# Kernel tuning notes

Measured on AMD Instinct MI355X. Metric: run time of the kernel, lower is better.

Reference implementation:

```python
import jax, jax.numpy as jnp
import numpy as np

PH = PW = 8
HEADS = 8
ADIM = 256
DH = ADIM // HEADS
N_KEYS = 3
CK, CV, CQ = 16, 32, 16
KS = 7
K_PDIM = PH * PW * CK   # 1024
V_PDIM = PH * PW * CV   # 2048
Q_PDIM = PH * PW * CQ   # 1024
MB_IN = N_KEYS * CV     # 96
MB_HID = 4 * MB_IN      # 384


def _to_patches(x):
    # b c (h ph) (w pw) -> b (h w) (ph pw c)
    b, c, H, W = x.shape
    h, w = H // PH, W // PW
    x = x.reshape(b, c, h, PH, w, PW).transpose(0, 2, 4, 3, 5, 1)
    return x.reshape(b, h * w, PH * PW * c)


def _layernorm(x, g, b):
    m = x.mean(-1, keepdims=True)
    v = x.var(-1, keepdims=True)
    return (x - m) * jax.lax.rsqrt(v + 1e-5) * g + b


def _embed(x, W1, b1, W2, b2):
    # NonLinearEmbedding: Linear -> GELU -> Linear
    return jax.nn.gelu(x @ W1 + b1) @ W2 + b2


def _to_heads(x):
    # b n (h d) -> b h n d
    b, n, hd = x.shape
    return x.reshape(b, n, HEADS, hd // HEADS).transpose(0, 2, 1, 3)


def _conv(x, w, b, groups, pad):
    y = jax.lax.conv_general_dilated(
        x, w, (1, 1), pad,
        dimension_numbers=('NCHW', 'OIHW', 'NCHW'),
        feature_group_count=groups)
    return y + b[None, :, None, None]


def _mbconv(x, w_exp, b_exp, w_dw, b_dw, w_proj, b_proj):
    # grouped 1x1 expand -> GELU -> depthwise kxk -> GELU -> grouped 1x1 project
    h = jax.nn.gelu(_conv(x, w_exp, b_exp, HEADS, 'VALID'))
    h = jax.nn.gelu(_conv(h, w_dw, b_dw, MB_HID, 'SAME'))
    return _conv(h, w_proj, b_proj, HEADS, 'VALID')


def setup_inputs() -> dict:
    key = jax.random.key(0)
    ks = jax.random.split(key, 24)
    B = 2
    key_sizes = [(256, 256), (192, 320), (128, 128)]
    query_sizes = [(256, 256), (192, 192)]
    s = 0.02
    inp = {}
    for i, (h, w) in enumerate(key_sizes):
        inp[f'keys_{i}'] = jax.random.normal(ks[i], (B, CK, h, w), jnp.float32)
        inp[f'values_{i}'] = jax.random.normal(ks[3 + i], (B, CV, h, w), jnp.float32)
    for i, (h, w) in enumerate(query_sizes):
        inp[f'queries_{i}'] = jax.random.normal(ks[6 + i], (B, CQ, h, w), jnp.float32)
    inp['ln_g'] = jnp.ones((V_PDIM,), jnp.float32)
    inp['ln_b'] = jnp.zeros((V_PDIM,), jnp.float32)
    inp['kW1'] = jax.random.normal(ks[8], (K_PDIM, ADIM), jnp.float32) * s
    inp['kb1'] = jnp.zeros((ADIM,), jnp.float32)
    inp['kW2'] = jax.random.normal(ks[9], (ADIM, ADIM), jnp.float32) * s
    inp['kb2'] = jnp.zeros((ADIM,), jnp.float32)
    inp['qW1'] = jax.random.normal(ks[10], (Q_PDIM, ADIM), jnp.float32) * s
    inp['qb1'] = jnp.zeros((ADIM,), jnp.float32)
    inp['qW2'] = jax.random.normal(ks[11], (ADIM, ADIM), jnp.float32) * s
    inp['qb2'] = jnp.zeros((ADIM,), jnp.float32)
    inp['w_exp'] = jax.random.normal(ks[12], (MB_HID, MB_IN // HEADS, 1, 1), jnp.float32) * s
    inp['b_exp'] = jnp.zeros((MB_HID,), jnp.float32)
    inp['w_dw'] = jax.random.normal(ks[13], (MB_HID, 1, KS, KS), jnp.float32) * s
    inp['b_dw'] = jnp.zeros((MB_HID,), jnp.float32)
    inp['w_proj'] = jax.random.normal(ks[14], (CV, MB_HID // HEADS, 1, 1), jnp.float32) * s
    inp['b_proj'] = jnp.zeros((CV,), jnp.float32)
    return inp


def reference(keys_0, keys_1, keys_2, values_0, values_1, values_2,
              queries_0, queries_1, ln_g, ln_b, kW1, kb1, kW2, kb2,
              qW1, qb1, qW2, qb2, w_exp, b_exp, w_dw, b_dw, w_proj, b_proj):
    keys = [keys_0, keys_1, keys_2]
    values = [values_0, values_1, values_2]
    queries = [queries_0, queries_1]
    # spatial sizes are already multiples of (PH, PW) -> pad_to_next_multiple is identity
    query_sizes = [q.shape[-2:] for q in queries]
    kp = [_to_patches(k) for k in keys]
    vp = [_to_patches(v) for v in values]
    qp = [_to_patches(q) for q in queries]
    nk = [p.shape[1] for p in kp]
    nq = [p.shape[1] for p in qp]
    k_seq = jnp.concatenate(kp, axis=1)               # (b, Nk, K_PDIM)
    v_seq = _layernorm(jnp.concatenate(vp, axis=1), ln_g, ln_b)  # (b, Nk, V_PDIM)
    q_seq = jnp.concatenate(qp, axis=1)               # (b, Nq, Q_PDIM)
    k_emb = _to_heads(_embed(k_seq, kW1, kb1, kW2, kb2))  # (b, h, Nk, DH)
    q_emb = _to_heads(_embed(q_seq, qW1, qb1, qW2, qb2))  # (b, h, Nq, DH)
    v_h = _to_heads(v_seq)                                # (b, h, Nk, dv)
    scale = jnp.asarray(1.0 / np.sqrt(DH), k_emb.dtype)
    attn = jnp.einsum('bhid,bhjd->bhij', q_emb, k_emb) * scale
    attn = jax.nn.softmax(attn, axis=-1)
    offs = np.cumsum([0] + nk)
    # per-source weighted values, stacked along a new source axis k
    weighted = jnp.stack(
        [attn[..., offs[i]:offs[i + 1]] @ v_h[:, :, offs[i]:offs[i + 1]]
         for i in range(N_KEYS)], axis=1)              # (b, k, h, Nq, dv)
    qoffs = np.cumsum([0] + nq)
    outs = []
    c = CV // HEADS
    for i, (qh, qw) in enumerate(query_sizes):
        v = weighted[:, :, :, qoffs[i]:qoffs[i + 1]]   # (b, k, hd, n, d)
        b, k, hd, n, d = v.shape
        h, w = qh // PH, qw // PW
        # b k hd (h w) (ph pw c) -> b (hd k c) (h ph) (w pw)
        v = v.reshape(b, k, hd, h, w, PH, PW, c).transpose(0, 2, 1, 7, 3, 5, 4, 6)
        v = v.reshape(b, hd * k * c, h * PH, w * PW)
        outs.append(_mbconv(v, w_exp, b_exp, w_dw, b_dw, w_proj, b_proj))
    return tuple(outs)
```

## Files before the change

### kernel.cpp

```cpp
#include <hip/hip_runtime.h>
#include <hip/hip_bf16.h>
#include <math.h>

typedef unsigned short bfu;
typedef __attribute__((ext_vector_type(8))) short short8v;
typedef __attribute__((ext_vector_type(4))) float f32x4;
typedef __attribute__((ext_vector_type(2))) float f32x2;

__device__ __forceinline__ float fast_rcp(float d) {
    float r = __builtin_amdgcn_rcpf(d);
    return r * fmaf(-d, r, 2.0f);
}
__device__ __forceinline__ f32x2 fma2(f32x2 a, f32x2 b, f32x2 c) {
    return __builtin_elementwise_fma(a, b, c);
}
__device__ __forceinline__ f32x2 splat2(float w) { return (f32x2){w, w}; }
__device__ __forceinline__ float gelu_f(float x) {
    float x3 = x * x * x;
    float e = __expf(1.5957691f * fmaf(0.044715f, x3, x));
    return x * e * __builtin_amdgcn_rcpf(e + 1.0f);
}
__device__ __forceinline__ f32x2 gelu2(f32x2 x) {
    f32x2 x3 = x * x * x;
    f32x2 z = fma2(splat2(0.044715f), x3, x) * 1.5957691f;
    f32x2 e = {__expf(z.x), __expf(z.y)};
    f32x2 d = e + 1.0f;
    f32x2 r = {__builtin_amdgcn_rcpf(d.x), __builtin_amdgcn_rcpf(d.y)};
    return x * e * r;
}
__device__ __forceinline__ float bf2f(bfu u) {
    union { float f; unsigned int i; } v; v.i = ((unsigned int)u) << 16; return v.f;
}
__device__ __forceinline__ bfu f2bf(float f) {
    union { float f; unsigned int i; } v; v.f = f;
    unsigned int r = v.i + 0x7fff + ((v.i >> 16) & 1);
    return (bfu)(r >> 16);
}
__device__ __forceinline__ float ldin(const void* p, size_t i, bool f32) {
    return f32 ? ((const float*)p)[i] : bf2f(((const bfu*)p)[i]);
}
__device__ __forceinline__ void stout(void* p, size_t i, float v, bool f32) {
    if (f32) ((float*)p)[i] = v;
    else     ((bfu*)p)[i] = f2bf(v);
}
__device__ __forceinline__ short8v ld_frag8(const bfu* p) {
    union { short8v v; ushort4 u[2]; } t;
    t.u[0] = *(const ushort4*)p;
    t.u[1] = *(const ushort4*)(p + 4);
    return t.v;
}

__global__ __launch_bounds__(256) void detect_kernel(const void* probe, int* flag) {
    __shared__ int red[4];
    const bfu* p = (const bfu*)probe;
    int tid = threadIdx.x;
    int insane = 0;
    for (int i = tid; i < 2048; i += 256) {
        unsigned e = (p[i] >> 7) & 0xFF;
        if (e >= 0xC0 || (e != 0 && e < 0x40)) insane++;
    }
    for (int o = 32; o > 0; o >>= 1) insane += __shfl_down(insane, o);
    if ((tid & 63) == 0) red[tid >> 6] = insane;
    __syncthreads();
    if (tid == 0) flag[0] = (red[0] + red[1] + red[2] + red[3] > 64) ? 1 : 0;
}

__global__ __launch_bounds__(256) void zero_out_kernel(bfu* __restrict__ out, int n) {
    int i = blockIdx.x * 256 + threadIdx.x;
    if (i < n) out[i] = 0;
}

__global__ __launch_bounds__(256) void wprep_kernel(
    const void* __restrict__ wexp, const void* __restrict__ bexp,
    const void* __restrict__ wdw, const void* __restrict__ bdw,
    const void* __restrict__ wproj, const void* __restrict__ bproj,
    const int* __restrict__ flag, float* __restrict__ wf)
{
    bool f32 = flag[0] != 0;
    int i = blockIdx.x * 256 + threadIdx.x;
    if (i < 4608)       wf[i] = ldin(wexp, i, f32);
    else if (i < 4992)  wf[i] = ldin(bexp, i - 4608, f32);
    else if (i < 23808) wf[i] = ldin(wdw, i - 4992, f32);
    else if (i < 24192) wf[i] = ldin(bdw, i - 23808, f32);
    else if (i < 25728) wf[i] = ldin(wproj, i - 24192, f32);
    else if (i < 25760) wf[i] = ldin(bproj, i - 25728, f32);
}

__global__ __launch_bounds__(256) void ln_stats_kernel(
    const void* __restrict__ v0, const void* __restrict__ v1, const void* __restrict__ v2,
    const int* __restrict__ flag, float* __restrict__ m_buf, float* __restrict__ i_buf)
{
    __shared__ float red[16];
    bool f32 = flag[0] != 0;
    int bid = blockIdx.x;
    int b = bid / 2240, n = bid - b * 2240;
    const void* src; int nl, wp, H, W;
    if (n < 1024)      { src = v0; nl = n;        wp = 32; H = 256; W = 256; }
    else if (n < 1984) { src = v1; nl = n - 1024; wp = 40; H = 192; W = 320; }
    else               { src = v2; nl = n - 1984; wp = 16; H = 128; W = 128; }
    int tid = threadIdx.x;
    int py = nl / wp, px = nl - py * wp;
    int ybase = py * 8, xbase = px * 8;
    float s1 = 0.f, s2 = 0.f;
    #pragma unroll
    for (int i = 0; i < 8; i++) {
        int j = tid + 256 * i;
        int ph = j >> 8, pw = (j >> 5) & 7, c = j & 31;
        float v = ldin(src, ((size_t)(b * 32 + c) * H + ybase + ph) * W + xbase + pw, f32);
        s1 += v; s2 = fmaf(v, v, s2);
    }
    for (int o = 32; o > 0; o >>= 1) { s1 += __shfl_down(s1, o); s2 += __shfl_down(s2, o); }
    int wid = tid >> 6;
    if ((tid & 63) == 0) { red[wid] = s1; red[8 + wid] = s2; }
    __syncthreads();
    if (tid == 0) {
        float a = red[0] + red[1] + red[2] + red[3];
        float q = red[8] + red[9] + red[10] + red[11];
        float m = a * (1.0f / 2048.0f);
        float var = q * (1.0f / 2048.0f) - m * m;
        m_buf[bid] = m;
        i_buf[bid] = 1.0f / sqrtf(var + 1e-5f);
    }
}

__global__ __launch_bounds__(256) void vstage_kernel(
    const void* __restrict__ v0, const void* __restrict__ v1, const void* __restrict__ v2,
    const void* __restrict__ g, const void* __restrict__ beta,
    const int* __restrict__ flag, bfu* __restrict__ out)
{
    __shared__ float red[16];
    __shared__ float mv[2];
    __shared__ __align__(16) bfu Ls[2048];
    bool f32 = flag[0] != 0;
    int bid = blockIdx.x;
    int b = bid / 2240, n = bid - b * 2240;
    const void* src; int nl, wpn, H, W;
    if (n < 1024)      { src = v0; nl = n;        wpn = 32; H = 256; W = 256; }
    else if (n < 1984) { src = v1; nl = n - 1024; wpn = 40; H = 192; W = 320; }
    else               { src = v2; nl = n - 1984; wpn = 16; H = 128; W = 128; }
    int tid = threadIdx.x;
    int py = nl / wpn, px = nl - py * wpn;
    int p = tid & 63;
    int c0 = tid >> 6;
    int y = py * 8 + (p >> 3), x = px * 8 + (p & 7);
    size_t HW = (size_t)H * W;
    size_t base = ((size_t)(b * 32 + c0) * H + y) * W + x;
    float vals[8];
    float s1 = 0.f, s2 = 0.f;
    #pragma unroll
    for (int i = 0; i < 8; i++) {
        float v = ldin(src, base + (size_t)(i << 2) * HW, f32);
        vals[i] = v; s1 += v; s2 = fmaf(v, v, s2);
    }
    for (int o = 32; o > 0; o >>= 1) { s1 += __shfl_down(s1, o); s2 += __shfl_down(s2, o); }
    int wid = tid >> 6;
    if ((tid & 63) == 0) { red[wid] = s1; red[8 + wid] = s2; }
    __syncthreads();
    if (tid == 0) {
        float a = red[0] + red[1] + red[2] + red[3];
        float q = red[8] + red[9] + red[10] + red[11];
        float m = a * (1.0f / 2048.0f);
        float var = q * (1.0f / 2048.0f) - m * m;
        mv[0] = m; mv[1] = 1.0f / sqrtf(var + 1e-5f);
    }
    __syncthreads();
    float m = mv[0], inv = mv[1];
    int jb = (p >> 3) * 256 + (p & 7) * 32 + c0;
    #pragma unroll
    for (int i = 0; i < 8; i++) {
        int j = jb + (i << 2);
        float o = (vals[i] - m) * inv * ldin(g, j, f32) + ldin(beta, j, f32);
        Ls[j] = f2bf(o);
    }
    __syncthreads();
    short8v* dst = (short8v*)(out + (size_t)bid * 2048);
    dst[tid] = ((const short8v*)Ls)[tid];
}

__global__ __launch_bounds__(256) void vtr_kernel(
    const bfu* __restrict__ vseq, bfu* __restrict__ vT)
{
    __shared__ __align__(16) bfu Ls[17408];
    int bid = blockIdx.x;
    int ch = bid % 35;
    int t = bid / 35;
    int h = t & 7, b = t >> 3;
    int c = threadIdx.x;
    const bfu* srcb = vseq + (((size_t)(b * 2240 + (ch << 6))) << 11) + (h << 8) + c;
    #pragma unroll
    for (int k4 = 0; k4 < 16; k4++) {
        ushort4 v;
        v.x = srcb[(size_t)(k4 * 4 + 0) << 11];
        v.y = srcb[(size_t)(k4 * 4 + 1) << 11];
        v.z = srcb[(size_t)(k4 * 4 + 2) << 11];
        v.w = srcb[(size_t)(k4 * 4 + 3) << 11];
        *(ushort4*)&Ls[c * 68 + k4 * 4] = v;
    }
    __syncthreads();
    short8v* dst = (short8v*)(vT + (size_t)((b * 8 + h) * 35 + ch) * 17408);
    const short8v* s = (const short8v*)Ls;
    #pragma unroll
    for (int r = 0; r < 8; r++) dst[(r << 8) + c] = s[(r << 8) + c];
    if (c < 128) dst[2048 + c] = s[2048 + c];
}

__global__ __launch_bounds__(256) void kstage_kernel(
    const void* __restrict__ k0, const void* __restrict__ k1, const void* __restrict__ k2,
    const void* __restrict__ q0, const void* __restrict__ q1,
    const int* __restrict__ flag, bfu* __restrict__ k_seq, bfu* __restrict__ q_seq)
{
    bool f32 = flag[0] != 0;
    int tid = threadIdx.x;
    int w = tid >> 6, l = tid & 63;
    int row = blockIdx.x * 4 + w;
    const void* src; int b, nl, wpn, H, W; bfu* dst;
    if (row < 4480) {
        b = row / 2240; int n = row - b * 2240;
        if (n < 1024)      { src = k0; nl = n;        wpn = 32; H = 256; W = 256; }
        else if (n < 1984) { src = k1; nl = n - 1024; wpn = 40; H = 192; W = 320; }
        else               { src = k2; nl = n - 1984; wpn = 16; H = 128; W = 128; }
        dst = k_seq + ((size_t)row << 10);
    } else {
        int r2 = row - 4480;
        b = r2 / 1600; int n = r2 - b * 1600;
        if (n < 1024)      { src = q0; nl = n;        wpn = 32; H = 256; W = 256; }
        else               { src = q1; nl = n - 1024; wpn = 24; H = 192; W = 192; }
        dst = q_seq + ((size_t)r2 << 10);
    }
    int py = nl / wpn, px = nl - py * wpn;
    int y = (py << 3) + (l >> 3), x = (px << 3) + (l & 7);
    size_t HW = (size_t)H * W;
    size_t base = ((size_t)(b * 16) * H + y) * W + x;
    bfu vals[16];
    #pragma unroll
    for (int c = 0; c < 16; c++) vals[c] = f2bf(ldin(src, base + c * HW, f32));
    bfu* dp = dst + (l << 4);
    *(ushort4*)(dp + 0)  = *(ushort4*)&vals[0];
    *(ushort4*)(dp + 4)  = *(ushort4*)&vals[4];
    *(ushort4*)(dp + 8)  = *(ushort4*)&vals[8];
    *(ushort4*)(dp + 12) = *(ushort4*)&vals[12];
}

__global__ __launch_bounds__(256) void wstage_kernel(
    const void* __restrict__ kW1, const void* __restrict__ qW1,
    const void* __restrict__ kW2, const void* __restrict__ qW2,
    const void* __restrict__ kb1, const void* __restrict__ qb1,
    const void* __restrict__ kb2, const void* __restrict__ qb2,
    const int* __restrict__ flag, bfu* __restrict__ WT, float* __restrict__ biasf)
{
    __shared__ float Ls[64][65];
    bool f32 = flag[0] != 0;
    int bid = blockIdx.x;
    int tid = threadIdx.x;
    if (bid == 160) {
        biasf[tid]       = ldin(kb1, tid, f32);
        biasf[256 + tid] = ldin(qb1, tid, f32);
        biasf[512 + tid] = ldin(kb2, tid, f32);
        biasf[768 + tid] = ldin(qb2, tid, f32);
        return;
    }
    const void* src; bfu* dst; int K, t;
    if (bid < 64)       { src = kW1; dst = WT;          K = 1024; t = bid; }
    else if (bid < 128) { src = qW1; dst = WT + 262144; K = 1024; t = bid - 64; }
    else if (bid < 144) { src = kW2; dst = WT + 524288; K = 256;  t = bid - 128; }
    else                { src = qW2; dst = WT + 589824; K = 256;  t = bid - 144; }
    int ktiles = K >> 6;
    int tk = t % ktiles, tc = t / ktiles;
    int k0 = tk << 6, c0 = tc << 6;
    int j = tid & 63, i0 = tid >> 6;
    #pragma unroll
    for (int p = 0; p < 16; p++) {
        int i = i0 + (p << 2);
        Ls[j][i] = ldin(src, (size_t)(k0 + i) * 256 + c0 + j, f32);
    }
    __syncthreads();
    #pragma unroll
    for (int p = 0; p < 16; p++) {
        int ci = i0 + (p << 2);
        dst[(size_t)(c0 + ci) * K + k0 + j] = f2bf(Ls[ci][j]);
    }
}

__global__ __launch_bounds__(256) void embed_mfma_kernel(
    const bfu* __restrict__ Ak, const bfu* __restrict__ Aq,
    const bfu* __restrict__ WTk, const bfu* __restrict__ WTq,
    const float* __restrict__ bk, const float* __restrict__ bq,
    bfu* __restrict__ Ck, bfu* __restrict__ Cq,
    int K, int gelu, int tiles0)
{
    int bid = blockIdx.x;
    int c0 = (bid & 3) << 6;
    int rt = bid >> 2;
    const bfu* A; const bfu* WT; const float* bias; bfu* C;
    int row0;
    if (rt < tiles0) { A = Ak; WT = WTk; bias = bk; C = Ck; row0 = rt << 6; }
    else             { A = Aq; WT = WTq; bias = bq; C = Cq; row0 = (rt - tiles0) << 6; }
    int tid = threadIdx.x;
    int w = tid >> 6, l = tid & 63;
    int l15 = l & 15, g = l >> 4;
    f32x4 zero4 = {0.f, 0.f, 0.f, 0.f};
    f32x4 acc[4] = {zero4, zero4, zero4, zero4};
    const bfu* wp = WT + (size_t)(c0 + (w << 4) + l15) * K + (g << 3);
    const bfu* ap = A + (size_t)(row0 + l15) * K + (g << 3);
    int nk = K >> 5;
    for (int kk = 0; kk < nk; kk++) {
        short8v af = ld_frag8(wp + (kk << 5));
        #pragma unroll
        for (int r2 = 0; r2 < 4; r2++) {
            short8v bf = ld_frag8(ap + (size_t)(r2 << 4) * K + (kk << 5));
            acc[r2] = __builtin_amdgcn_mfma_f32_16x16x32_bf16(af, bf, acc[r2], 0, 0, 0);
        }
    }
    int colb = c0 + (w << 4) + (g << 2);
    float4 bb = *(const float4*)&bias[colb];
    #pragma unroll
    for (int r2 = 0; r2 < 4; r2++) {
        float v0 = acc[r2][0] + bb.x;
        float v1 = acc[r2][1] + bb.y;
        float v2 = acc[r2][2] + bb.z;
        float v3 = acc[r2][3] + bb.w;
        if (gelu) { v0 = gelu_f(v0); v1 = gelu_f(v1); v2 = gelu_f(v2); v3 = gelu_f(v3); }
        ushort4 o;
        o.x = f2bf(v0); o.y = f2bf(v1); o.z = f2bf(v2); o.w = f2bf(v3);
        *(ushort4*)(C + (size_t)(row0 + (r2 << 4) + l15) * 256 + colb) = o;
    }
}

__global__ __launch_bounds__(256) void embed1_kernel(
    const void* __restrict__ k0, const void* __restrict__ k1, const void* __restrict__ k2,
    const void* __restrict__ q0, const void* __restrict__ q1,
    const void* __restrict__ kW1, const void* __restrict__ kb1,
    const void* __restrict__ qW1, const void* __restrict__ qb1,
    const int* __restrict__ flag,
    bfu* __restrict__ k_hid, bfu* __restrict__ q_hid)
{
    __shared__ float As[16][68];
    __shared__ float Bs[16][68];
    bool f32 = flag[0] != 0;
    int bid = blockIdx.x;
    int colBase = (bid & 3) << 6;
    int rt = bid >> 2;
    const void* Wm; const void* bias; bfu* C;
    int rowBase, isK;
    if (rt < 70) { isK = 1; Wm = kW1; bias = kb1; C = k_hid; rowBase = rt << 6; }
    else         { isK = 0; Wm = qW1; bias = qb1; C = q_hid; rowBase = (rt - 70) << 6; }
    int tid = threadIdx.x;
    int tx = tid & 15, ty = tid >> 4;
    int arow = tid >> 2, akq = (tid & 3) << 2;
    int brow = tid >> 4, bcol = (tid & 15) << 2;
    int row = rowBase + arow;
    int nTot = isK ? 2240 : 1600;
    int b = row / nTot, n = row - b * nTot;
    const void* src; int nl, wp, H, W;
    if (isK) {
        if (n < 1024)      { src = k0; nl = n;        wp = 32; H = 256; W = 256; }
        else if (n < 1984) { src = k1; nl = n - 1024; wp = 40; H = 192; W = 320; }
        else               { src = k2; nl = n - 1984; wp = 16; H = 128; W = 128; }
    } else {
        if (n < 1024)      { src = q0; nl = n;        wp = 32; H = 256; W = 256; }
        else               { src = q1; nl = n - 1024; wp = 24; H = 192; W = 192; }
    }
    int py = nl / wp, px = nl - py * wp;
    int ybase = py << 3, xbase = px << 3;
    size_t HW = (size_t)H * W;
    size_t abase = (size_t)(b * 16 + akq) * HW;
    size_t wbase = (size_t)brow * 256 + colBase + bcol;
    float acc[4][4] = {};
    for (int k0i = 0; k0i < 1024; k0i += 16) {
        int j = k0i + akq;
        int ph = j >> 7, pw = (j >> 4) & 7;
        size_t ai = abase + (size_t)(ybase + ph) * W + xbase + pw;
        As[akq + 0][arow] = ldin(src, ai, f32);
        As[akq + 1][arow] = ldin(src, ai + HW, f32);
        As[akq + 2][arow] = ldin(src, ai + 2 * HW, f32);
        As[akq + 3][arow] = ldin(src, ai + 3 * HW, f32);
        size_t wo = wbase + (size_t)k0i * 256;
        #pragma unroll
        for (int t = 0; t < 4; t++) Bs[brow][bcol + t] = ldin(Wm, wo + t, f32);
        __syncthreads();
        #pragma unroll
        for (int kk = 0; kk < 16; kk++) {
            float4 a4 = *(const float4*)&As[kk][ty << 2];
            float4 p0 = *(const float4*)&Bs[kk][tx << 2];
            float ar[4] = {a4.x, a4.y, a4.z, a4.w};
            float br[4] = {p0.x, p0.y, p0.z, p0.w};
            #pragma unroll
            for (int rr = 0; rr < 4; rr++)
                #pragma unroll
                for (int i = 0; i < 4; i++)
                    acc[rr][i] = fmaf(ar[rr], br[i], acc[rr][i]);
        }
        __syncthreads();
    }
    int cg = colBase + (tx << 2);
    float bbr[4];
    #pragma unroll
    for (int i = 0; i < 4; i++) bbr[i] = ldin(bias, cg + i, f32);
    #pragma unroll
    for (int rr = 0; rr < 4; rr++) {
        ushort4 o;
        o.x = f2bf(gelu_f(acc[rr][0] + bbr[0]));
        o.y = f2bf(gelu_f(acc[rr][1] + bbr[1]));
        o.z = f2bf(gelu_f(acc[rr][2] + bbr[2]));
        o.w = f2bf(gelu_f(acc[rr][3] + bbr[3]));
        *(ushort4*)(&C[(size_t)(rowBase + (ty << 2) + rr) * 256 + cg]) = o;
    }
}

__global__ __launch_bounds__(256) void embed2_kernel(
    const bfu* __restrict__ A0, const void* __restrict__ W0, const void* __restrict__ bias0,
    bfu* __restrict__ C0, int tiles0,
    const bfu* __restrict__ A1, const void* __restrict__ W1, const void* __restrict__ bias1,
    bfu* __restrict__ C1, const int* __restrict__ flag)
{
    __shared__ float As[16][68];
    __shared__ float Bs[16][68];
    bool f32 = flag[0] != 0;
    int bid = blockIdx.x;
    int colBase = (bid & 3) << 6;
    int rt = bid >> 2;
    const bfu* A; const void* Wm; const void* bias; bfu* C;
    int rowBase;
    if (rt < tiles0) { A = A0; Wm = W0; bias = bias0; C = C0; rowBase = rt << 6; }
    else             { A = A1; Wm = W1; bias = bias1; C = C1; rowBase = (rt - tiles0) << 6; }
    int tid = threadIdx.x;
    int tx = tid & 15, ty = tid >> 4;
    int arow = tid >> 2, akq = (tid & 3) << 2;
    int brow = tid >> 4, bcol = (tid & 15) << 2;
    const bfu* Ap = A + (size_t)(rowBase + arow) * 256 + akq;
    size_t wbase = (size_t)brow * 256 + colBase + bcol;
    float acc[4][4] = {};
    for (int k0 = 0; k0 < 256; k0 += 16) {
        ushort4 av = *(const ushort4*)(Ap + k0);
        As[akq + 0][arow] = bf2f(av.x);
        As[akq + 1][arow] = bf2f(av.y);
        As[akq + 2][arow] = bf2f(av.z);
        As[akq + 3][arow] = bf2f(av.w);
        size_t wo = wbase + (size_t)k0 * 256;
        #pragma unroll
        for (int t = 0; t < 4; t++) Bs[brow][bcol + t] = ldin(Wm, wo + t, f32);
        __syncthreads();
        #pragma unroll
        for (int kk = 0; kk < 16; kk++) {
            float4 a4 = *(const float4*)&As[kk][ty << 2];
            float4 p0 = *(const float4*)&Bs[kk][tx << 2];
            float ar[4] = {a4.x, a4.y, a4.z, a4.w};
            float br[4] = {p0.x, p0.y, p0.z, p0.w};
            #pragma unroll
            for (int rr = 0; rr < 4; rr++)
                #pragma unroll
                for (int i = 0; i < 4; i++)
                    acc[rr][i] = fmaf(ar[rr], br[i], acc[rr][i]);
        }
        __syncthreads();
    }
    int cg = colBase + (tx << 2);
    float bbr[4];
    #pragma unroll
    for (int i = 0; i < 4; i++) bbr[i] = ldin(bias, cg + i, f32);
    #pragma unroll
    for (int rr = 0; rr < 4; rr++) {
        ushort4 o;
        o.x = f2bf(acc[rr][0] + bbr[0]);
        o.y = f2bf(acc[rr][1] + bbr[1]);
        o.z = f2bf(acc[rr][2] + bbr[2]);
        o.w = f2bf(acc[rr][3] + bbr[3]);
        *(ushort4*)(&C[(size_t)(rowBase + (ty << 2) + rr) * 256 + cg]) = o;
    }
}

__global__ __launch_bounds__(256) void attn_mfma_kernel(
    const bfu* __restrict__ qe, const bfu* __restrict__ ke,
    const bfu* __restrict__ vT,
    bfu* __restrict__ wbuf, float* __restrict__ lbuf, int h0, int hs)
{
    __shared__ __align__(16) bfu Vs[17408];
    __shared__ __align__(16) bfu Ps[2176];
    __shared__ float red[4][16];
    int bid = blockIdx.x;
    int qtile = bid % 50;
    int t = bid / 50;
    int hh = t % hs, b = t / hs;
    int h = h0 + hh;
    int n0 = qtile << 5;
    int tid = threadIdx.x;
    int w = tid >> 6, l = tid & 63;
    int l15 = l & 15, g = l >> 4;
    int wqt = w >> 1;
    int wkp = (w & 1) << 1;

    short8v qf = *(const short8v*)(qe + (((size_t)(b * 1600 + n0 + (wqt << 4) + l15)) << 8) + (h << 5) + (g << 3));

    f32x4 zero4 = {0.f, 0.f, 0.f, 0.f};
    f32x4 acc[2][4];
    #pragma unroll
    for (int i = 0; i < 2; i++)
        #pragma unroll
        for (int j = 0; j < 4; j++) acc[i][j] = zero4;
    float rs = 0.f;
    const float scale = 0.17677669529663687f;

    const short8v* vbase = (const short8v*)(vT + (size_t)((b * 8 + h) * 35) * 17408);
    short8v* VsV = (short8v*)Vs;

    for (int ch = 0; ch < 35; ch++) {
        const short8v* src = vbase + (size_t)ch * 2176;
        #pragma unroll
        for (int r = 0; r < 8; r++) VsV[(r << 8) + tid] = src[(r << 8) + tid];
        if (tid < 128) VsV[2048 + tid] = src[2048 + tid];
        #pragma unroll
        for (int j = 0; j < 2; j++) {
            int ktile = wkp + j;
            short8v kf = *(const short8v*)(ke + (((size_t)(b * 2240 + (ch << 6) + (ktile << 4) + l15)) << 8) + (h << 5) + (g << 3));
            f32x4 st = __builtin_amdgcn_mfma_f32_16x16x32_bf16(kf, qf, zero4, 0, 0, 0);
            float p0 = __expf(st[0] * scale);
            float p1 = __expf(st[1] * scale);
            float p2 = __expf(st[2] * scale);
            float p3 = __expf(st[3] * scale);
            rs += (p0 + p1) + (p2 + p3);
            ushort4 pk;
            pk.x = f2bf(p0); pk.y = f2bf(p1); pk.z = f2bf(p2); pk.w = f2bf(p3);
            *(ushort4*)&Ps[((wqt << 4) + l15) * 68 + (ktile << 4) + (g << 2)] = pk;
        }
        __syncthreads();
        #pragma unroll
        for (int kt = 0; kt < 2; kt++) {
            short8v a0 = ld_frag8(&Ps[l15 * 68 + (kt << 5) + (g << 3)]);
            short8v a1 = ld_frag8(&Ps[(16 + l15) * 68 + (kt << 5) + (g << 3)]);
            #pragma unroll
            for (int nt = 0; nt < 4; nt++) {
                int ntg = (w << 2) + nt;
                short8v bf = ld_frag8(&Vs[((ntg << 4) + l15) * 68 + (kt << 5) + (g << 3)]);
                acc[0][nt] = __builtin_amdgcn_mfma_f32_16x16x32_bf16(a0, bf, acc[0][nt], 0, 0, 0);
                acc[1][nt] = __builtin_amdgcn_mfma_f32_16x16x32_bf16(a1, bf, acc[1][nt], 0, 0, 0);
            }
        }
        __syncthreads();
        if (ch == 15 || ch == 30 || ch == 34) {
            int srcid = (ch == 15) ? 0 : (ch == 30 ? 1 : 2);
            bfu* wb = wbuf + ((size_t)((b * hs + hh) * 3 + srcid) * 1600 + n0) * 256 + (w << 6) + l15;
            #pragma unroll
            for (int q2 = 0; q2 < 2; q2++)
                #pragma unroll
                for (int nt = 0; nt < 4; nt++) {
                    #pragma unroll
                    for (int r = 0; r < 4; r++) {
                        wb[(size_t)((q2 << 4) + (g << 2) + r) * 256 + (nt << 4)] = f2bf(acc[q2][nt][r]);
                        acc[q2][nt][r] = 0.f;
                    }
                }
        }
    }
    rs += __shfl_xor(rs, 16);
    rs += __shfl_xor(rs, 32);
    if (l < 16) red[w][l15] = rs;
    __syncthreads();
    if (tid < 32) {
        int q2 = tid >> 4;
        float tot = red[q2 << 1][tid & 15] + red[(q2 << 1) + 1][tid & 15];
        lbuf[(size_t)(b * 8 + h) * 1600 + n0 + tid] = tot;
    }
}

__global__ __launch_bounds__(256) void attn_kernel(
    const bfu* __restrict__ qe, const bfu* __restrict__ ke,
    const bfu* __restrict__ vseq,
    const void* __restrict__ v0, const void* __restrict__ v1, const void* __restrict__ v2,
    const void* __restrict__ ln_g, const void* __restrict__ ln_b,
    const float* __restrict__ m_buf, const float* __restrict__ i_buf,
    const int* __restrict__ flag,
    bfu* __restrict__ wbuf, float* __restrict__ lbuf, int h0, int hs)
{
    __shared__ float Qs[32][36];
    __shared__ float Ks[32][37];
    __shared__ float Ps2[32][37];
    __shared__ float Vls[32][260];
    __shared__ float gbg[256];
    __shared__ float gbb[256];
    bool f32 = flag[0] != 0;
    int bid = blockIdx.x;
    int qt = bid % 50;
    int t = bid / 50;
    int hh = t % hs;
    int b = t / hs;
    int h = h0 + hh;
    int n0 = qt << 5;
    int tid = threadIdx.x;
    int tx = tid & 15, ty = tid >> 4;
    if (!vseq) {
        gbg[tid] = ldin(ln_g, h * 256 + tid, f32);
        gbb[tid] = ldin(ln_b, h * 256 + tid, f32);
    }
    {
        int r = tid >> 3, d0 = (tid & 7) << 2;
        const bfu* qp = qe + (size_t)(b * 1600 + n0 + r) * 256 + (h << 5) + d0;
        ushort4 a = *(const ushort4*)qp;
        Qs[r][d0 + 0] = bf2f(a.x); Qs[r][d0 + 1] = bf2f(a.y);
        Qs[r][d0 + 2] = bf2f(a.z); Qs[r][d0 + 3] = bf2f(a.w);
    }
    float lreg = 0.f;
    float acc[2][4][4] = {};
    const float scale = 0.17677669529663687f;
    int kvrow = tid >> 3, kq = (tid & 7) << 2;
    const bfu* kbase = ke + (size_t)(b * 2240 + kvrow) * 256 + (h << 5) + kq;
    const bfu* vsbase = vseq ? vseq + (size_t)(b * 2240 + kvrow) * 2048 + (h << 8) + kq : nullptr;
    for (int ch = 0; ch < 70; ch++) {
        {
            ushort4 kv = *(const ushort4*)(kbase + (size_t)ch * 8192);
            Ks[kvrow][kq + 0] = bf2f(kv.x);
            Ks[kvrow][kq + 1] = bf2f(kv.y);
            Ks[kvrow][kq + 2] = bf2f(kv.z);
            Ks[kvrow][kq + 3] = bf2f(kv.w);
        }
        if (vseq) {
            #pragma unroll
            for (int i = 0; i < 8; i++) {
                ushort4 u = *(const ushort4*)(vsbase + (size_t)ch * 65536 + (i << 5));
                int d = (i << 5) + kq;
                Vls[kvrow][d + 0] = bf2f(u.x);
                Vls[kvrow][d + 1] = bf2f(u.y);
                Vls[kvrow][d + 2] = bf2f(u.z);
                Vls[kvrow][d + 3] = bf2f(u.w);
            }
        } else {
            int n = ch * 32 + kvrow;
            const void* vsrc; int nl, wp, H, W;
            if (n < 1024)      { vsrc = v0; nl = n;        wp = 32; H = 256; W = 256; }
            else if (n < 1984) { vsrc = v1; nl = n - 1024; wp = 40; H = 192; W = 320; }
            else               { vsrc = v2; nl = n - 1984; wp = 16; H = 128; W = 128; }
            int py = nl / wp, px = nl - py * wp;
            int y = py * 8 + h, xb = px * 8;
            float m = m_buf[b * 2240 + n];
            float inv = i_buf[b * 2240 + n];
            size_t HW = (size_t)H * W;
            size_t vbi = ((size_t)(b * 32 + kq) * H + y) * W + xb;
            #pragma unroll
            for (int i = 0; i < 8; i++) {
                int d = (i << 5) + kq;
                float t0 = (ldin(vsrc, vbi + i, f32) - m) * inv;
                float t1 = (ldin(vsrc, vbi + i + HW, f32) - m) * inv;
                float t2 = (ldin(vsrc, vbi + i + 2 * HW, f32) - m) * inv;
                float t3 = (ldin(vsrc, vbi + i + 3 * HW, f32) - m) * inv;
                Vls[kvrow][d + 0] = fmaf(t0, gbg[d + 0], gbb[d + 0]);
                Vls[kvrow][d + 1] = fmaf(t1, gbg[d + 1], gbb[d + 1]);
                Vls[kvrow][d + 2] = fmaf(t2, gbg[d + 2], gbb[d + 2]);
                Vls[kvrow][d + 3] = fmaf(t3, gbg[d + 3], gbb[d + 3]);
            }
        }
        __syncthreads();
        float s[2][2] = {};
        #pragma unroll 8
        for (int d = 0; d < 32; d++) {
            float k0v = Ks[(tx << 1) + 0][d];
            float k1v = Ks[(tx << 1) + 1][d];
            #pragma unroll
            for (int rr = 0; rr < 2; rr++) {
                float qv = Qs[(ty << 1) + rr][d];
                s[rr][0] = fmaf(qv, k0v, s[rr][0]);
                s[rr][1] = fmaf(qv, k1v, s[rr][1]);
            }
        }
        #pragma unroll
        for (int rr = 0; rr < 2; rr++) {
            Ps2[(ty << 1) + rr][(tx << 1) + 0] = __expf(s[rr][0] * scale);
            Ps2[(ty << 1) + rr][(tx << 1) + 1] = __expf(s[rr][1] * scale);
        }
        __syncthreads();
        if (tid < 32) {
            float t2 = 0.f;
            #pragma unroll
            for (int jj = 0; jj < 32; jj++) t2 += Ps2[tid][jj];
            lreg += t2;
        }
        #pragma unroll 4
        for (int j = 0; j < 32; j++) {
            float4 w0 = *(const float4*)&Vls[j][(tx << 2)];
            float4 w1 = *(const float4*)&Vls[j][64 + (tx << 2)];
            float4 w2 = *(const float4*)&Vls[j][128 + (tx << 2)];
            float4 w3 = *(const float4*)&Vls[j][192 + (tx << 2)];
            #pragma unroll
            for (int rr = 0; rr < 2; rr++) {
                float p = Ps2[(ty << 1) + rr][j];
                acc[rr][0][0] = fmaf(p, w0.x, acc[rr][0][0]);
                acc[rr][0][1] = fmaf(p, w0.y, acc[rr][0][1]);
                acc[rr][0][2] = fmaf(p, w0.z, acc[rr][0][2]);
                acc[rr][0][3] = fmaf(p, w0.w, acc[rr][0][3]);
                acc[rr][1][0] = fmaf(p, w1.x, acc[rr][1][0]);
                acc[rr][1][1] = fmaf(p, w1.y, acc[rr][1][1]);
                acc[rr][1][2] = fmaf(p, w1.z, acc[rr][1][2]);
                acc[rr][1][3] = fmaf(p, w1.w, acc[rr][1][3]);
                acc[rr][2][0] = fmaf(p, w2.x, acc[rr][2][0]);
                acc[rr][2][1] = fmaf(p, w2.y, acc[rr][2][1]);
                acc[rr][2][2] = fmaf(p, w2.z, acc[rr][2][2]);
                acc[rr][2][3] = fmaf(p, w2.w, acc[rr][2][3]);
                acc[rr][3][0] = fmaf(p, w3.x, acc[rr][3][0]);
                acc[rr][3][1] = fmaf(p, w3.y, acc[rr][3][1]);
                acc[rr][3][2] = fmaf(p, w3.z, acc[rr][3][2]);
                acc[rr][3][3] = fmaf(p, w3.w, acc[rr][3][3]);
            }
        }
        __syncthreads();
        if (ch == 31 || ch == 61 || ch == 69) {
            int src = (ch == 31) ? 0 : (ch == 61 ? 1 : 2);
            bfu* wb = wbuf + (size_t)(((b * hs + hh) * 3 + src) * 1600 + n0 + (ty << 1)) * 256 + (tx << 2);
            #pragma unroll
            for (int rr = 0; rr < 2; rr++) {
                #pragma unroll
                for (int q = 0; q < 4; q++) {
                    ushort4 u;
                    u.x = f2bf(acc[rr][q][0]); u.y = f2bf(acc[rr][q][1]);
                    u.z = f2bf(acc[rr][q][2]); u.w = f2bf(acc[rr][q][3]);
                    *(ushort4*)(wb + (size_t)rr * 256 + (q << 6)) = u;
                    acc[rr][q][0] = acc[rr][q][1] = acc[rr][q][2] = acc[rr][q][3] = 0.f;
                }
            }
        }
    }
    if (tid < 32) lbuf[(size_t)(b * 8 + h) * 1600 + n0 + tid] = lreg;
}

__global__ __launch_bounds__(256) void mbconv_kernel(
    const bfu* __restrict__ wbuf, const float* __restrict__ lbuf,
    const float* __restrict__ wf, const int* __restrict__ flag,
    void* __restrict__ out, size_t out_off, int H, int W, int n_base,
    int tilesX, int tilesY, int h0, int hs)
{
    __shared__ __align__(16) float h1s[8][528];
    __shared__ float h2s[256][9];
    bool f32o = flag[0] != 0;
    const float* wexp_f  = wf;
    const float* bexp_f  = wf + 4608;
    const float* wdw_f   = wf + 4992;
    const float* bdw_f   = wf + 23808;
    const float* wproj_f = wf + 24192;
    const float* bproj_f = wf + 25728;
    int bid = blockIdx.x;
    int gi = bid % hs;
    int t2b = bid / hs;
    int tilesTot = tilesX * tilesY;
    int b = t2b / tilesTot;
    int rem = t2b - b * tilesTot;
    int tY = rem / tilesX, tX = rem - tY * tilesX;
    int gy0 = tY << 4, gx0 = tX << 4;
    int wp = W >> 3;
    int tid = threadIdx.x;
    int wu = __builtin_amdgcn_readfirstlane(tid >> 6);
    int l = tid & 63;
    int doy = ((l >> 3) & 7) << 1;
    int dox = (l & 7) << 1;
    int g = h0 + gi;

    f32x2 xsr2[12];
    #pragma unroll
    for (int ci = 0; ci < 12; ci++) xsr2[ci] = (f32x2){0.f, 0.f};
    int pa0 = 0, pa1 = 0; bool pv0 = false, pv1 = false;
    bool act = tid < 242;
    if (act) {
        #pragma unroll
        for (int j = 0; j < 2; j++) {
            int p = tid * 2 + j;
            int py = p / 22, px = p - py * 22;
            int y = gy0 - 3 + py, x = gx0 - 3 + px;
            bool valid = (y >= 0) && (y < H) && (x >= 0) && (x < W);
            if (j == 0) { pa0 = py * 24 + px; pv0 = valid; }
            else        { pa1 = py * 24 + px; pv1 = valid; }
            if (valid) {
                int n = n_base + (y >> 3) * wp + (x >> 3);
                float invl = fast_rcp(lbuf[(size_t)(b * 8 + g) * 1600 + n]);
                int d = ((y & 7) << 5) + ((x & 7) << 2);
                const bfu* src = wbuf + ((size_t)((b * hs + gi) * 3) * 1600 + n) * 256 + d;
                #pragma unroll
                for (int k = 0; k < 3; k++) {
                    ushort4 u = *(const ushort4*)(src + (size_t)k * 409600);
                    if (j == 0) {
                        xsr2[k * 4 + 0].x = bf2f(u.x) * invl;
                        xsr2[k * 4 + 1].x = bf2f(u.y) * invl;
                        xsr2[k * 4 + 2].x = bf2f(u.z) * invl;
                        xsr2[k * 4 + 3].x = bf2f(u.w) * invl;
                    } else {
                        xsr2[k * 4 + 0].y = bf2f(u.x) * invl;
                        xsr2[k * 4 + 1].y = bf2f(u.y) * invl;
                        xsr2[k * 4 + 2].y = bf2f(u.z) * invl;
                        xsr2[k * 4 + 3].y = bf2f(u.w) * invl;
                    }
                }
            }
        }
    }

    float oacc[4] = {0.f, 0.f, 0.f, 0.f};
    for (int chunk = 0; chunk < 6; chunk++) {
        int hc0 = g * 48 + chunk * 8;
        __syncthreads();
        if (act) {
            #pragma unroll
            for (int c = 0; c < 8; c++) {
                const float* we = &wexp_f[(size_t)(hc0 + c) * 12];
                f32x2 a = splat2(bexp_f[hc0 + c]);
                #pragma unroll
                for (int ci = 0; ci < 12; ci++)
                    a = fma2(splat2(we[ci]), xsr2[ci], a);
                f32x2 gv = gelu2(a);
                h1s[c][pa0] = pv0 ? gv.x : 0.f;
                h1s[c][pa1] = pv1 ? gv.y : 0.f;
            }
        }
        __syncthreads();
        #pragma unroll
        for (int c2 = 0; c2 < 2; c2++) {
            int ch = wu + (c2 << 2);
            const float* wd = &wdw_f[(size_t)(hc0 + ch) * 49];
            float bd = bdw_f[hc0 + ch];
            f32x2 a2v0 = splat2(bd);
            f32x2 a2v1 = splat2(bd);
            #pragma unroll
            for (int r = 0; r < 8; r++) {
                const f32x2* rp = (const f32x2*)&h1s[ch][(doy + r) * 24 + dox];
                f32x2 p0 = rp[0], p1 = rp[1], p2 = rp[2], p3 = rp[3];
                f32x2 q0 = {p0.y, p1.x}, q1 = {p1.y, p2.x}, q2 = {p2.y, p3.x};
                f32x2 win[7] = {p0, q0, p1, q1, p2, q2, p3};
                if (r <= 6) {
                    const float* wk = &wd[r * 7];
                    #pragma unroll
                    for (int kx = 0; kx < 7; kx++)
                        a2v0 = fma2(splat2(wk[kx]), win[kx], a2v0);
                }
                if (r >= 1) {
                    const float* wk = &wd[(r - 1) * 7];
                    #pragma unroll
                    for (int kx = 0; kx < 7; kx++)
                        a2v1 = fma2(splat2(wk[kx]), win[kx], a2v1);
                }
            }
            f32x2 g0 = gelu2(a2v0), g1 = gelu2(a2v1);
            h2s[(doy + 0) * 16 + dox + 0][ch] = g0.x;
            h2s[(doy + 0) * 16 + dox + 1][ch] = g0.y;
            h2s[(doy + 1) * 16 + dox + 0][ch] = g1.x;
            h2s[(doy + 1) * 16 + dox + 1][ch] = g1.y;
        }
        __syncthreads();
        #pragma unroll
        for (int c = 0; c < 8; c++) {
            float hv = h2s[tid][c];
            #pragma unroll
            for (int oc = 0; oc < 4; oc++)
                oacc[oc] = fmaf(hv, wproj_f[(size_t)(g * 4 + oc) * 48 + chunk * 8 + c], oacc[oc]);
        }
    }
    int yy = tid >> 4, xx = tid & 15;
    #pragma unroll
    for (int oc = 0; oc < 4; oc++) {
        stout(out, out_off + ((size_t)(b * 32 + g * 4 + oc) * H + gy0 + yy) * W + gx0 + xx,
              oacc[oc] + bproj_f[g * 4 + oc], f32o);
    }
}

extern "C" void kernel_launch(void* const* d_in, const int* in_sizes, int n_in,
                              void* d_out, int out_size, void* d_ws, size_t ws_size,
                              hipStream_t stream)
{
    const void *keys0, *keys1, *keys2, *vals0, *vals1, *vals2;
    keys0 = d_in[0];
    if (in_sizes[1] == 4194304) {
        vals0 = d_in[1]; keys1 = d_in[2]; vals1 = d_in[3]; keys2 = d_in[4]; vals2 = d_in[5];
    } else {
        keys1 = d_in[1]; keys2 = d_in[2]; vals0 = d_in[3]; vals1 = d_in[4]; vals2 = d_in[5];
    }
    const void* qrys0  = d_in[6];
    const void* qrys1  = d_in[7];
    const void* ln_g   = d_in[8];
    const void* ln_b   = d_in[9];
    const void* kW1    = d_in[10];
    const void* kb1    = d_in[11];
    const void* kW2    = d_in[12];
    const void* kb2    = d_in[13];
    const void* qW1    = d_in[14];
    const void* qb1    = d_in[15];
    const void* qW2    = d_in[16];
    const void* qb2    = d_in[17];
    const void* w_exp  = d_in[18];
    const void* b_exp  = d_in[19];
    const void* w_dw   = d_in[20];
    const void* b_dw   = d_in[21];
    const void* w_proj = d_in[22];
    const void* b_proj = d_in[23];

    char* base = (char*)d_ws;
    int*   flag  = (int*)base;
    bfu*   k_emb = (bfu*)(base + 64);
    bfu*   q_emb = (bfu*)(base + 64 + 2293760);
    float* l_buf = (float*)(base + 64 + 3932160);
    float* m_buf = (float*)(base + 64 + 4034560);
    float* i_buf = (float*)(base + 64 + 4052480);
    const size_t FIXED0 = 4070464ULL;
    float* w_f   = (float*)(base + FIXED0);
    const size_t FIXEDN = FIXED0 + 103040ULL;
    const size_t VSEQB = 18350080ULL;
    const size_t VTB   = 19496960ULL;
    const size_t RX    = FIXEDN + VTB;

    const size_t EMB = 20975616ULL;
    const size_t need8 = RX + 39321600ULL;
    const size_t need4 = RX + EMB;
    const size_t need2 = RX + EMB;

    detect_kernel<<<1, 256, 0, stream>>>(keys0, flag);
    wprep_kernel<<<101, 256, 0, stream>>>(w_exp, b_exp, w_dw, b_dw, w_proj, b_proj, flag, w_f);

    if (ws_size >= need2) {
        int hs = (ws_size >= need8) ? 8 : (ws_size >= need4 ? 4 : 2);
        bfu*   vT    = (bfu*)(base + FIXEDN);
        bfu*   v_seq = (bfu*)(base + RX);
        bfu*   k_seq = (bfu*)(base + RX);
        bfu*   q_seq = (bfu*)(base + RX + 9175040);
        bfu*   WTb   = (bfu*)(base + RX + 15728640);
        float* biasf = (float*)(base + RX + 17039360);
        bfu*   k_hid = (bfu*)(base + RX + 17043456);
        bfu*   q_hid = (bfu*)(base + RX + 19337216);
        bfu*   w_buf = (bfu*)(base + RX);

        vstage_kernel<<<4480, 256, 0, stream>>>(vals0, vals1, vals2, ln_g, ln_b, flag, v_seq);
        vtr_kernel<<<560, 256, 0, stream>>>(v_seq, vT);
        kstage_kernel<<<1920, 256, 0, stream>>>(keys0, keys1, keys2, qrys0, qrys1,
                                                flag, k_seq, q_seq);
        wstage_kernel<<<161, 256, 0, stream>>>(kW1, qW1, kW2, qW2, kb1, qb1, kb2, qb2,
                                               flag, WTb, biasf);
        embed_mfma_kernel<<<480, 256, 0, stream>>>(k_seq, q_seq, WTb, WTb + 262144,
                                                   biasf, biasf + 256, k_hid, q_hid,
                                                   1024, 1, 70);
        embed_mfma_kernel<<<480, 256, 0, stream>>>(k_hid, q_hid, WTb + 524288, WTb + 589824,
                                                   biasf + 512, biasf + 768, k_emb, q_emb,
                                                   256, 0, 70);
        for (int h0 = 0; h0 < 8; h0 += hs) {
            attn_mfma_kernel<<<2 * hs * 50, 256, 0, stream>>>(
                q_emb, k_emb, vT, w_buf, l_buf, h0, hs);
            mbconv_kernel<<<2 * 256 * hs, 256, 0, stream>>>(
                w_buf, l_buf, w_f, flag,
                d_out, 0, 256, 256, 0, 16, 16, h0, hs);
            mbconv_kernel<<<2 * 144 * hs, 256, 0, stream>>>(
                w_buf, l_buf, w_f, flag,
                d_out, 4194304, 192, 192, 1024, 12, 12, h0, hs);
        }
        return;
    }

    int hs;
    if      (ws_size >= FIXEDN + 8ULL * 4915200ULL) hs = 8;
    else if (ws_size >= FIXEDN + 4ULL * 4915200ULL) hs = 4;
    else if (ws_size >= FIXEDN + 2ULL * 4915200ULL) hs = 2;
    else if (ws_size >= FIXEDN + 1ULL * 4915200ULL) hs = 1;
    else {
        zero_out_kernel<<<(out_size + 255) / 256, 256, 0, stream>>>((bfu*)d_out, out_size);
        return;
    }
    char* rest  = base + FIXEDN;
    bfu*  k_hid = (bfu*)rest;
    bfu*  q_hid = (bfu*)(rest + 2293760);
    bfu*  w_buf = (bfu*)rest;

    ln_stats_kernel<<<4480, 256, 0, stream>>>(vals0, vals1, vals2, flag, m_buf, i_buf);
    embed1_kernel<<<480, 256, 0, stream>>>(keys0, keys1, keys2, qrys0, qrys1,
                                           kW1, kb1, qW1, qb1, flag, k_hid, q_hid);
    embed2_kernel<<<480, 256, 0, stream>>>(k_hid, kW2, kb2, k_emb, 70,
                                           q_hid, qW2, qb2, q_emb, flag);
    for (int h0 = 0; h0 < 8; h0 += hs) {
        attn_kernel<<<2 * hs * 50, 256, 0, stream>>>(
            q_emb, k_emb, nullptr, vals0, vals1, vals2, ln_g, ln_b, m_buf, i_buf, flag,
            w_buf, l_buf, h0, hs);
        mbconv_kernel<<<2 * 256 * hs, 256, 0, stream>>>(
            w_buf, l_buf, w_f, flag,
            d_out, 0, 256, 256, 0, 16, 16, h0, hs);
        mbconv_kernel<<<2 * 144 * hs, 256, 0, stream>>>(
            w_buf, l_buf, w_f, flag,
            d_out, 4194304, 192, 192, 1024, 12, 12, h0, hs);
    }
}
```

Measured before the change: 551.4 us.

## Split attention across key sources into separate blocks with partial row sums

```diff
diff --git a/kernel.cpp b/kernel.cpp
--- a/kernel.cpp
+++ b/kernel.cpp
@@ -6,6 +6,7 @@
 typedef __attribute__((ext_vector_type(8))) short short8v;
 typedef __attribute__((ext_vector_type(4))) float f32x4;
 typedef __attribute__((ext_vector_type(2))) float f32x2;
+typedef struct __attribute__((packed)) { float x, y; } f2p;
 
 __device__ __forceinline__ float fast_rcp(float d) {
     float r = __builtin_amdgcn_rcpf(d);
@@ -469,10 +470,10 @@
     }
 }
 
-__global__ __launch_bounds__(256) void attn_mfma_kernel(
+__global__ __launch_bounds__(256) void attn_mfma3_kernel(
     const bfu* __restrict__ qe, const bfu* __restrict__ ke,
     const bfu* __restrict__ vT,
-    bfu* __restrict__ wbuf, float* __restrict__ lbuf, int h0, int hs)
+    bfu* __restrict__ wbuf, float* __restrict__ lbuf3, int h0, int hs)
 {
     __shared__ __align__(16) bfu Vs[17408];
     __shared__ __align__(16) bfu Ps[2176];
@@ -480,9 +481,13 @@
     int bid = blockIdx.x;
     int qtile = bid % 50;
     int t = bid / 50;
-    int hh = t % hs, b = t / hs;
+    int src3 = t % 3;
+    int t2 = t / 3;
+    int hh = t2 % hs, b = t2 / hs;
     int h = h0 + hh;
     int n0 = qtile << 5;
+    int lo = (src3 == 0) ? 0 : (src3 == 1 ? 16 : 31);
+    int hi = (src3 == 0) ? 16 : (src3 == 1 ? 31 : 35);
     int tid = threadIdx.x;
     int w = tid >> 6, l = tid & 63;
     int l15 = l & 15, g = l >> 4;
@@ -503,7 +508,7 @@
     const short8v* vbase = (const short8v*)(vT + (size_t)((b * 8 + h) * 35) * 17408);
     short8v* VsV = (short8v*)Vs;
 
-    for (int ch = 0; ch < 35; ch++) {
+    for (int ch = lo; ch < hi; ch++) {
         const short8v* src = vbase + (size_t)ch * 2176;
         #pragma unroll
         for (int r = 0; r < 8; r++) VsV[(r << 8) + tid] = src[(r << 8) + tid];
@@ -536,20 +541,16 @@
             }
         }
         __syncthreads();
-        if (ch == 15 || ch == 30 || ch == 34) {
-            int srcid = (ch == 15) ? 0 : (ch == 30 ? 1 : 2);
-            bfu* wb = wbuf + ((size_t)((b * hs + hh) * 3 + srcid) * 1600 + n0) * 256 + (w << 6) + l15;
-            #pragma unroll
-            for (int q2 = 0; q2 < 2; q2++)
+    }
+    {
+        bfu* wb = wbuf + ((size_t)((b * hs + hh) * 3 + src3) * 1600 + n0) * 256 + (w << 6) + l15;
+        #pragma unroll
+        for (int q2 = 0; q2 < 2; q2++)
+            #pragma unroll
+            for (int nt = 0; nt < 4; nt++)
                 #pragma unroll
-                for (int nt = 0; nt < 4; nt++) {
-                    #pragma unroll
-                    for (int r = 0; r < 4; r++) {
-                        wb[(size_t)((q2 << 4) + (g << 2) + r) * 256 + (nt << 4)] = f2bf(acc[q2][nt][r]);
-                        acc[q2][nt][r] = 0.f;
-                    }
-                }
-        }
+                for (int r = 0; r < 4; r++)
+                    wb[(size_t)((q2 << 4) + (g << 2) + r) * 256 + (nt << 4)] = f2bf(acc[q2][nt][r]);
     }
     rs += __shfl_xor(rs, 16);
     rs += __shfl_xor(rs, 32);
@@ -558,7 +559,7 @@
     if (tid < 32) {
         int q2 = tid >> 4;
         float tot = red[q2 << 1][tid & 15] + red[(q2 << 1) + 1][tid & 15];
-        lbuf[(size_t)(b * 8 + h) * 1600 + n0 + tid] = tot;
+        lbuf3[src3 * 25600 + (size_t)(b * 8 + h) * 1600 + n0 + tid] = tot;
     }
 }
 
@@ -720,7 +721,7 @@
 }
 
 __global__ __launch_bounds__(256) void mbconv_kernel(
-    const bfu* __restrict__ wbuf, const float* __restrict__ lbuf,
+    const bfu* __restrict__ wbuf, const float* __restrict__ lbuf3,
     const float* __restrict__ wf, const int* __restrict__ flag,
     void* __restrict__ out, size_t out_off, int H, int W, int n_base,
     int tilesX, int tilesY, int h0, int hs)
@@ -766,7 +767,8 @@
             else        { pa1 = py * 24 + px; pv1 = valid; }
             if (valid) {
                 int n = n_base + (y >> 3) * wp + (x >> 3);
-                float invl = fast_rcp(lbuf[(size_t)(b * 8 + g) * 1600 + n]);
+                int li = (b * 8 + g) * 1600 + n;
+                float invl = fast_rcp(lbuf3[li] + lbuf3[25600 + li] + lbuf3[51200 + li]);
                 int d = ((y & 7) << 5) + ((x & 7) << 2);
                 const bfu* src = wbuf + ((size_t)((b * hs + gi) * 3) * 1600 + n) * 256 + d;
                 #pragma unroll
@@ -815,9 +817,15 @@
             f32x2 a2v1 = splat2(bd);
             #pragma unroll
             for (int r = 0; r < 8; r++) {
-                const f32x2* rp = (const f32x2*)&h1s[ch][(doy + r) * 24 + dox];
-                f32x2 p0 = rp[0], p1 = rp[1], p2 = rp[2], p3 = rp[3];
-                f32x2 q0 = {p0.y, p1.x}, q1 = {p1.y, p2.x}, q2 = {p2.y, p3.x};
+                const float* hrow = &h1s[ch][(doy + r) * 24 + dox];
+                f32x2 p0 = *(const f32x2*)hrow;
+                f32x2 p1 = *(const f32x2*)(hrow + 2);
+                f32x2 p2 = *(const f32x2*)(hrow + 4);
+                f32x2 p3 = *(const f32x2*)(hrow + 6);
+                const f2p* qp = (const f2p*)(hrow + 1);
+                f32x2 q0 = {qp[0].x, qp[0].y};
+                f32x2 q1 = {qp[1].x, qp[1].y};
+                f32x2 q2 = {qp[2].x, qp[2].y};
                 f32x2 win[7] = {p0, q0, p1, q1, p2, q2, p3};
                 if (r <= 6) {
                     const float* wk = &wd[r * 7];
@@ -889,26 +897,24 @@
     int*   flag  = (int*)base;
     bfu*   k_emb = (bfu*)(base + 64);
     bfu*   q_emb = (bfu*)(base + 64 + 2293760);
-    float* l_buf = (float*)(base + 64 + 3932160);
     float* m_buf = (float*)(base + 64 + 4034560);
     float* i_buf = (float*)(base + 64 + 4052480);
     const size_t FIXED0 = 4070464ULL;
     float* w_f   = (float*)(base + FIXED0);
-    const size_t FIXEDN = FIXED0 + 103040ULL;
-    const size_t VSEQB = 18350080ULL;
-    const size_t VTB   = 19496960ULL;
-    const size_t RX    = FIXEDN + VTB;
+    float* lbuf3 = (float*)(base + FIXED0 + 103040);
+    const size_t FIXEDN = FIXED0 + 103040ULL + 307200ULL;
+    const size_t VTB    = 19496960ULL;
+    const size_t RX     = FIXEDN + VTB;
 
     const size_t EMB = 20975616ULL;
     const size_t need8 = RX + 39321600ULL;
     const size_t need4 = RX + EMB;
-    const size_t need2 = RX + EMB;
 
     detect_kernel<<<1, 256, 0, stream>>>(keys0, flag);
     wprep_kernel<<<101, 256, 0, stream>>>(w_exp, b_exp, w_dw, b_dw, w_proj, b_proj, flag, w_f);
 
-    if (ws_size >= need2) {
-        int hs = (ws_size >= need8) ? 8 : (ws_size >= need4 ? 4 : 2);
+    if (ws_size >= need4) {
+        int hs = (ws_size >= need8) ? 8 : 4;
         bfu*   vT    = (bfu*)(base + FIXEDN);
         bfu*   v_seq = (bfu*)(base + RX);
         bfu*   k_seq = (bfu*)(base + RX);
@@ -932,13 +938,13 @@
                                                    biasf + 512, biasf + 768, k_emb, q_emb,
                                                    256, 0, 70);
         for (int h0 = 0; h0 < 8; h0 += hs) {
-            attn_mfma_kernel<<<2 * hs * 50, 256, 0, stream>>>(
-                q_emb, k_emb, vT, w_buf, l_buf, h0, hs);
+            attn_mfma3_kernel<<<3 * 2 * hs * 50, 256, 0, stream>>>(
+                q_emb, k_emb, vT, w_buf, lbuf3, h0, hs);
             mbconv_kernel<<<2 * 256 * hs, 256, 0, stream>>>(
-                w_buf, l_buf, w_f, flag,
+                w_buf, lbuf3, w_f, flag,
                 d_out, 0, 256, 256, 0, 16, 16, h0, hs);
             mbconv_kernel<<<2 * 144 * hs, 256, 0, stream>>>(
-                w_buf, l_buf, w_f, flag,
+                w_buf, lbuf3, w_f, flag,
                 d_out, 4194304, 192, 192, 1024, 12, 12, h0, hs);
         }
         return;
@@ -958,6 +964,7 @@
     bfu*  q_hid = (bfu*)(rest + 2293760);
     bfu*  w_buf = (bfu*)rest;
 
+    zero_out_kernel<<<400, 256, 0, stream>>>((bfu*)(lbuf3 + 25600), 102400);
     ln_stats_kernel<<<4480, 256, 0, stream>>>(vals0, vals1, vals2, flag, m_buf, i_buf);
     embed1_kernel<<<480, 256, 0, stream>>>(keys0, keys1, keys2, qrys0, qrys1,
                                            kW1, kb1, qW1, qb1, flag, k_hid, q_hid);
@@ -966,12 +973,12 @@
     for (int h0 = 0; h0 < 8; h0 += hs) {
         attn_kernel<<<2 * hs * 50, 256, 0, stream>>>(
             q_emb, k_emb, nullptr, vals0, vals1, vals2, ln_g, ln_b, m_buf, i_buf, flag,
-            w_buf, l_buf, h0, hs);
+            w_buf, lbuf3, h0, hs);
         mbconv_kernel<<<2 * 256 * hs, 256, 0, stream>>>(
-            w_buf, l_buf, w_f, flag,
+            w_buf, lbuf3, w_f, flag,
             d_out, 0, 256, 256, 0, 16, 16, h0, hs);
         mbconv_kernel<<<2 * 144 * hs, 256, 0, stream>>>(
-            w_buf, l_buf, w_f, flag,
+            w_buf, lbuf3, w_f, flag,
             d_out, 4194304, 192, 192, 1024, 12, 12, h0, hs);
     }
 }
```

Result: no change. 548.3 us (-0.6%).
